# Kernel tuning notes

Measured on AMD Instinct MI355X. Metric: run time of the kernel, lower is better.

## Reference

```python
import jax, jax.numpy as jnp
import numpy as np

POOL_RATIO = 0.25
ROUTING_NUM = 3
B, N, D, H = 32, 2048, 512, 512


def setup_inputs() -> dict:
    key = jax.random.key(0)
    k_x, k_adj, k_w = jax.random.split(key, 3)
    x = jax.random.normal(k_x, (B, N, D), dtype=jnp.float32)
    # variable node counts per graph; row 0 uses all N nodes so max_cluster is static
    rng = np.random.default_rng(0)
    lens = np.full(B, N, dtype=np.int64)
    lens[1:] = rng.integers(N // 2, N + 1, size=B - 1)
    mask_np = (np.arange(N)[None, :] < lens[:, None])  # [B,N] bool
    mask = jnp.asarray(mask_np)
    # sparse-ish random adjacency, zeroed outside the node mask
    adj = (jax.random.uniform(k_adj, (B, N, N)) < 0.01).astype(jnp.float32)
    m = mask.astype(jnp.float32)
    adj = adj * m[:, None, :] * m[:, :, None]
    W = jax.random.normal(k_w, (D, H), dtype=jnp.float32) * 0.02
    b = jnp.zeros((H,), dtype=jnp.float32)
    return {"x": x, "adj": adj, "W": W, "b": b, "mask": mask}


def masked_softmax(s, m):
    # m: bool broadcastable to s; masked entries -> exactly 0 probability
    s = jnp.where(m, s, jnp.float32(-1e9))
    return jax.nn.softmax(s, axis=-1) * m


def squash(s):
    # squash along last (feature) dim, as in torch sum(dim=2) on [B,C,H]
    mag_sq = jnp.sum(s * s, axis=-1, keepdims=True)
    mag = jnp.sqrt(mag_sq)
    return mag_sq / (1.0 + mag_sq) * (s / mag)


def reference(x, adj, W, b, mask):
    fmask = mask.astype(x.dtype)
    node_num = fmask.sum(axis=1)                               # [B]
    cluster_num = jnp.floor(node_num * POOL_RATIO).astype(jnp.int32)
    max_cluster = int(x.shape[1] * POOL_RATIO)                 # static (row 0 has N nodes)
    cmask = jnp.arange(max_cluster)[None, :] < cluster_num[:, None]  # [B,C] bool
    cm = cmask[:, None, :]                                     # [B,1,C]
    # embed: dense GCN layer  z = relu(adj @ x @ W + b)  -> [B,N,H]
    z = jax.nn.relu(jnp.einsum('bnm,bmd,dh->bnh', adj, x, W) + b)
    s = jax.random.normal(jax.random.key(42), (x.shape[0], x.shape[1], max_cluster), dtype=x.dtype)
    for _ in range(ROUTING_NUM):
        s = masked_softmax(s, cm)                              # [B,N,C]
        xnext = squash(jnp.einsum('bnc,bnh->bch', s, z))       # [B,C,H]
        s = s + jnp.einsum('bnh,bch->bnc', z, xnext)           # routing update
    return masked_softmax(s, cm)
```

## Files before the change

### kernel.cpp

```cpp
#include <hip/hip_runtime.h>
#include <cstdint>
#include <cstddef>

#define NB 32
#define NN 2048
#define ND 512
#define NH 512
#define NC 512
#define ROWS (NB*NN)

typedef __attribute__((ext_vector_type(8))) short short8v;
typedef __attribute__((ext_vector_type(4))) float f32x4;

#define MFMA16(a,b,c) __builtin_amdgcn_mfma_f32_16x16x32_bf16((a),(b),(c),0,0,0)

typedef const __attribute__((address_space(1))) unsigned int* gas_t;
typedef __attribute__((address_space(3))) unsigned int* las_t;

__device__ __forceinline__ void gload16(const void* g, void* l){
  __builtin_amdgcn_global_load_lds((gas_t)g, (las_t)l, 16, 0, 0);
}

__device__ __forceinline__ void fsplit(float v, unsigned short& h, unsigned short& l){
  unsigned u = __float_as_uint(v);
  unsigned hb = (u + 0x7FFFu + ((u>>16)&1u)) >> 16;
  float hf = __uint_as_float(hb<<16);
  float r = v - hf;
  unsigned ur = __float_as_uint(r);
  l = (unsigned short)((ur + 0x7FFFu + ((ur>>16)&1u)) >> 16);
  h = (unsigned short)hb;
}

__device__ __forceinline__ unsigned rotl32(unsigned x, int d){ return (x<<d)|(x>>(32-d)); }

__device__ __forceinline__ unsigned threefry_xor(unsigned k0, unsigned k1, unsigned c0, unsigned c1){
  unsigned ks2 = 0x1BD11BDAu ^ k0 ^ k1;
  unsigned x0 = c0 + k0, x1 = c1 + k1;
#define TF_RND(r) { x0 += x1; x1 = rotl32(x1,(r)); x1 ^= x0; }
  TF_RND(13) TF_RND(15) TF_RND(26) TF_RND(6)
  x0 += k1;  x1 += ks2 + 1u;
  TF_RND(17) TF_RND(29) TF_RND(16) TF_RND(24)
  x0 += ks2; x1 += k0 + 2u;
  TF_RND(13) TF_RND(15) TF_RND(26) TF_RND(6)
  x0 += k0;  x1 += k1 + 3u;
  TF_RND(17) TF_RND(29) TF_RND(16) TF_RND(24)
  x0 += k1;  x1 += ks2 + 4u;
  TF_RND(13) TF_RND(15) TF_RND(26) TF_RND(6)
  x0 += ks2; x1 += k0 + 5u;
#undef TF_RND
  return x0 ^ x1;
}

__device__ __forceinline__ float bits_to_normal(unsigned bits){
  float f = __uint_as_float((bits >> 9) | 0x3f800000u) - 1.0f;
  const float lo = -0.99999994f;
  float u = fmaxf(lo, fmaf(f, 2.0f, lo));
  float w = -log1pf(-(u*u));
  float p;
  if (w < 5.0f){
    w -= 2.5f;
    p =            2.81022636e-08f;
    p = fmaf(p, w, 3.43273939e-07f);
    p = fmaf(p, w, -3.5233877e-06f);
    p = fmaf(p, w, -4.39150654e-06f);
    p = fmaf(p, w, 0.00021858087f);
    p = fmaf(p, w, -0.00125372503f);
    p = fmaf(p, w, -0.00417768164f);
    p = fmaf(p, w, 0.246640727f);
    p = fmaf(p, w, 1.50140941f);
  } else {
    w = sqrtf(w) - 3.0f;
    p =            -0.000200214257f;
    p = fmaf(p, w, 0.000100950558f);
    p = fmaf(p, w, 0.00134934322f);
    p = fmaf(p, w, -0.00367342844f);
    p = fmaf(p, w, 0.00573950773f);
    p = fmaf(p, w, -0.0076224613f);
    p = fmaf(p, w, 0.00943887047f);
    p = fmaf(p, w, 1.00167406f);
    p = fmaf(p, w, 2.83297682f);
  }
  return 1.4142135623730951f * (p * u);
}

__global__ void __launch_bounds__(256) rng_kernel(float* __restrict__ s){
  unsigned i = blockIdx.x * 256u + threadIdx.x;
  s[i] = bits_to_normal(threefry_xor(0u, 42u, 0u, i));
}

__global__ void __launch_bounds__(256) counts_kernel(const unsigned char* __restrict__ mraw,
                                                     int* __restrict__ cnum){
  __shared__ int red[256];
  int b = blockIdx.x, tid = threadIdx.x;
  unsigned char b0 = mraw[0], b1 = mraw[1];
  int cnt = 0;
  if (b0 == 1 && b1 == 1){
    const unsigned char* p = mraw + (size_t)b * NN;
    for (int i = tid; i < NN; i += 256) cnt += (p[i] != 0);
  } else if (b0 == 1){
    const int* p = (const int*)mraw + (size_t)b * NN;
    for (int i = tid; i < NN; i += 256) cnt += (p[i] != 0);
  } else {
    const float* p = (const float*)mraw + (size_t)b * NN;
    for (int i = tid; i < NN; i += 256) cnt += (p[i] != 0.0f);
  }
  red[tid] = cnt; __syncthreads();
  for (int off = 128; off; off >>= 1){ if (tid < off) red[tid] += red[tid+off]; __syncthreads(); }
  if (tid == 0) cnum[b] = red[0] >> 2;
}

__global__ void __launch_bounds__(256) spmm_kernel(const float* __restrict__ adj,
                                                   const float* __restrict__ x,
                                                   unsigned short* __restrict__ yh,
                                                   unsigned short* __restrict__ yl){
  __shared__ int   idxs[NN];
  __shared__ float vals[NN];
  __shared__ int   scan[256];
  int row = blockIdx.x;
  int b = row >> 11;
  int tid = threadIdx.x;
  const float* arow = adj + (size_t)row * NN;
  float v[8];
  *(float4*)&v[0] = *(const float4*)(arow + tid*8);
  *(float4*)&v[4] = *(const float4*)(arow + tid*8 + 4);
  int lc = 0;
  #pragma unroll
  for (int j=0;j<8;j++) lc += (v[j] != 0.0f);
  scan[tid] = lc; __syncthreads();
  for (int off=1; off<256; off<<=1){
    int t = (tid >= off) ? scan[tid-off] : 0;
    __syncthreads();
    scan[tid] += t;
    __syncthreads();
  }
  int pos = scan[tid] - lc;
  int total = scan[255];
  #pragma unroll
  for (int j=0;j<8;j++){
    if (v[j] != 0.0f){ idxs[pos] = tid*8 + j; vals[pos] = v[j]; pos++; }
  }
  __syncthreads();
  float acc0 = 0.f, acc1 = 0.f;
  const float* xb = x + (size_t)b * NN * ND;
  for (int j=0;j<total;j++){
    int m = idxs[j]; float a = vals[j];
    acc0 = fmaf(a, xb[(size_t)m*ND + tid      ], acc0);
    acc1 = fmaf(a, xb[(size_t)m*ND + tid + 256], acc1);
  }
  unsigned short h,l;
  size_t base = (size_t)row * ND;
  fsplit(acc0,h,l); yh[base+tid]=h;     yl[base+tid]=l;
  fsplit(acc1,h,l); yh[base+tid+256]=h; yl[base+tid+256]=l;
}

__global__ void __launch_bounds__(256) wsplit_kernel(const float* __restrict__ W,
                                                     unsigned short* __restrict__ WTh,
                                                     unsigned short* __restrict__ WTl){
  __shared__ float t[32][33];
  int bx = blockIdx.x, by = blockIdx.y;
  int x = threadIdx.x & 31, y = threadIdx.x >> 5;
  for (int yy=y; yy<32; yy+=8) t[yy][x] = W[(size_t)(bx*32+yy)*512 + by*32 + x];
  __syncthreads();
  for (int yy=y; yy<32; yy+=8){
    float v = t[x][yy];
    unsigned short h,l; fsplit(v,h,l);
    size_t idx = (size_t)(by*32+yy)*512 + bx*32 + x;
    WTh[idx]=h; WTl[idx]=l;
  }
}

template<bool SPLIT>
__global__ void __launch_bounds__(256) softmax_kernel(float* __restrict__ s,
                                                      unsigned short* __restrict__ sh,
                                                      unsigned short* __restrict__ sl,
                                                      const int* __restrict__ cnum){
  int row  = blockIdx.x*4 + (threadIdx.x >> 6);
  int lane = threadIdx.x & 63;
  int b = row >> 11;
  int Kc = cnum[b];
  float* p = s + (size_t)row * NC;
  float4 v0 = *(const float4*)(p + lane*4);
  float4 v1 = *(const float4*)(p + lane*4 + 256);
  float e[8] = {v0.x,v0.y,v0.z,v0.w,v1.x,v1.y,v1.z,v1.w};
  float m = -3.0e38f;
  #pragma unroll
  for (int j=0;j<8;j++){
    int c = (j<4) ? lane*4 + j : lane*4 + 252 + j;
    if (c < Kc) m = fmaxf(m, e[j]);
  }
  #pragma unroll
  for (int off=32; off; off>>=1) m = fmaxf(m, __shfl_xor(m, off, 64));
  float r[8]; float sum = 0.f;
  #pragma unroll
  for (int j=0;j<8;j++){
    int c = (j<4) ? lane*4 + j : lane*4 + 252 + j;
    r[j] = (c < Kc) ? expf(e[j] - m) : 0.0f;
    sum += r[j];
  }
  #pragma unroll
  for (int off=32; off; off>>=1) sum += __shfl_xor(sum, off, 64);
  float inv = 1.0f / sum;
  #pragma unroll
  for (int j=0;j<8;j++) r[j] *= inv;
  *(float4*)(p + lane*4)       = make_float4(r[0],r[1],r[2],r[3]);
  *(float4*)(p + lane*4 + 256) = make_float4(r[4],r[5],r[6],r[7]);
  if constexpr (SPLIT){
    unsigned long long ph=0, pl=0, qh=0, ql=0;
    #pragma unroll
    for (int j=0;j<4;j++){
      unsigned short h,l;
      fsplit(r[j],h,l);
      ph |= (unsigned long long)h << (16*j);  pl |= (unsigned long long)l << (16*j);
      fsplit(r[4+j],h,l);
      qh |= (unsigned long long)h << (16*j);  ql |= (unsigned long long)l << (16*j);
    }
    size_t base = (size_t)row * NC + lane*4;
    *(unsigned long long*)(sh + base)       = ph;
    *(unsigned long long*)(sl + base)       = pl;
    *(unsigned long long*)(sh + base + 256) = qh;
    *(unsigned long long*)(sl + base + 256) = ql;
  }
}

template<int EPI>
__global__ void __launch_bounds__(512,2) gemm256_kernel(
    const unsigned short* __restrict__ Ah, const unsigned short* __restrict__ Al,
    const unsigned short* __restrict__ Bh, const unsigned short* __restrict__ Bl,
    unsigned short* __restrict__ OutH, unsigned short* __restrict__ OutL,
    float* __restrict__ Cf, const float* __restrict__ S2,
    const float* __restrict__ bias, const float* __restrict__ scale,
    int K, long sA, long sB, long sC)
{
  __shared__ __align__(16) unsigned char smem[131072];
  int bz = blockIdx.z;
  Ah += (size_t)bz*sA; Al += (size_t)bz*sA;
  Bh += (size_t)bz*sB; Bl += (size_t)bz*sB;
  if constexpr (EPI==2){ Cf += (size_t)bz*sC; S2 += (size_t)bz*sC; scale += (size_t)bz*NC; }
  int m0 = blockIdx.x*256, n0 = blockIdx.y*256;
  int tid = threadIdx.x;
  int l = tid & 63, wid = tid >> 6;
  int wr = wid >> 2, wc = wid & 3;
  int lr = l & 15, lk = l >> 4;

  int offA[8], offB[4];
  #pragma unroll
  for (int i=0;i<8;i++){
    int ra = wr*128 + i*16 + lr;
    offA[i] = ra*64 + ((lk ^ ((ra>>1)&3))<<4);
  }
  #pragma unroll
  for (int j=0;j<4;j++){
    int rb = wc*64 + j*16 + lr;
    offB[j] = rb*64 + ((lk ^ ((rb>>1)&3))<<4);
  }

  int srow = tid >> 2;
  int gslot = (tid & 3) ^ ((srow>>1)&3);
  const unsigned short* gA0 = Ah + (size_t)(m0 +       srow)*512 + gslot*8;
  const unsigned short* gA1 = Ah + (size_t)(m0 + 128 + srow)*512 + gslot*8;
  const unsigned short* gA2 = Al + (size_t)(m0 +       srow)*512 + gslot*8;
  const unsigned short* gA3 = Al + (size_t)(m0 + 128 + srow)*512 + gslot*8;
  const unsigned short* gB0 = Bh + (size_t)(n0 +       srow)*512 + gslot*8;
  const unsigned short* gB1 = Bh + (size_t)(n0 + 128 + srow)*512 + gslot*8;
  const unsigned short* gB2 = Bl + (size_t)(n0 +       srow)*512 + gslot*8;
  const unsigned short* gB3 = Bl + (size_t)(n0 + 128 + srow)*512 + gslot*8;

  f32x4 acc[8][4] = {};

#define STAGE256(buf, k0) { \
    unsigned char* db = smem + (buf)*65536 + wid*1024; \
    gload16(gA0 + (k0), db);          gload16(gA1 + (k0), db + 8192); \
    gload16(gA2 + (k0), db + 16384);  gload16(gA3 + (k0), db + 24576); \
    gload16(gB0 + (k0), db + 32768);  gload16(gB1 + (k0), db + 40960); \
    gload16(gB2 + (k0), db + 49152);  gload16(gB3 + (k0), db + 57344); }

  STAGE256(0, 0)
  __syncthreads();
  int KT = K >> 5;
  for (int t = 0; t < KT; ++t){
    if (t+1 < KT) STAGE256((t+1)&1, (t+1)*32)
    const unsigned char* base = smem + (t&1)*65536;
    short8v ah[8], bh[4], bl[4];
    #pragma unroll
    for (int i=0;i<8;i++) ah[i] = *(const short8v*)(base + offA[i]);
    #pragma unroll
    for (int j=0;j<4;j++){
      bh[j] = *(const short8v*)(base + 32768 + offB[j]);
      bl[j] = *(const short8v*)(base + 49152 + offB[j]);
    }
    #pragma unroll
    for (int i=0;i<8;i++)
      #pragma unroll
      for (int j=0;j<4;j++) acc[i][j] = MFMA16(ah[i], bh[j], acc[i][j]);
    #pragma unroll
    for (int i=0;i<8;i++)
      #pragma unroll
      for (int j=0;j<4;j++) acc[i][j] = MFMA16(ah[i], bl[j], acc[i][j]);
    #pragma unroll
    for (int i=0;i<8;i++){
      short8v al = *(const short8v*)(base + 16384 + offA[i]);
      #pragma unroll
      for (int j=0;j<4;j++) acc[i][j] = MFMA16(al, bh[j], acc[i][j]);
    }
    __syncthreads();
  }
#undef STAGE256

  float aux[4];
  #pragma unroll
  for (int j=0;j<4;j++){
    int gcol = n0 + wc*64 + j*16 + lr;
    if constexpr (EPI==1) aux[j] = bias[gcol];
    if constexpr (EPI==2) aux[j] = scale[gcol];
  }
  #pragma unroll
  for (int i=0;i<8;i++){
    #pragma unroll
    for (int r=0;r<4;r++){
      int grow = m0 + wr*128 + i*16 + lk*4 + r;
      size_t rowb = (size_t)grow*512 + n0 + wc*64 + lr;
      #pragma unroll
      for (int j=0;j<4;j++){
        float v = acc[i][j][r];
        if constexpr (EPI==1){
          v = fmaxf(v + aux[j], 0.f);
          unsigned short h,lo2; fsplit(v,h,lo2);
          OutH[rowb + j*16] = h; OutL[rowb + j*16] = lo2;
        } else {
          Cf[rowb + j*16] = S2[rowb + j*16] + aux[j]*v;
        }
      }
    }
  }
}

__global__ void __launch_bounds__(512,2) gemmT256_kernel(
    const unsigned short* __restrict__ Ah, const unsigned short* __restrict__ Al,
    const unsigned short* __restrict__ Bh, const unsigned short* __restrict__ Bl,
    unsigned short* __restrict__ OutH, unsigned short* __restrict__ OutL,
    float* __restrict__ parts, int K)
{
  __shared__ __align__(16) unsigned char smem[98304];
  int bz = blockIdx.z;
  size_t boff = (size_t)bz * NN * 512;
  Ah += boff; Al += boff; Bh += boff; Bl += boff;
  int m0 = blockIdx.x*256, n0 = blockIdx.y*128;
  int tid = threadIdx.x;
  int l = tid & 63, wid = tid >> 6;
  int wr = wid >> 2, wc = wid & 3;
  int lr = l & 15, lk = l >> 4;

  int offA[8], offB[2];
  #pragma unroll
  for (int i=0;i<8;i++){
    int ra = wr*128 + i*16 + lr;
    offA[i] = ra*64 + ((lk ^ ((ra>>1)&3) ^ ((ra>>3)&3))<<4);
  }
  #pragma unroll
  for (int j=0;j<2;j++){
    int rb = wc*32 + j*16 + lr;
    offB[j] = rb*64 + ((lk ^ ((rb>>1)&3) ^ ((rb>>3)&3))<<4);
  }

  int np  = tid & 15;
  int seg = tid >> 4;
  f32x4 acc[8][2] = {};

  short8v ra0h, ra1h, ra0l, ra1l, rb0h, rb1h, rb0l, rb1l;
  int have_b = (tid < 256);

#define TLOAD(k0) { \
    size_t ga = (size_t)((k0) + 2*np)*512 + m0 + seg*8; \
    ra0h = *(const short8v*)(Ah + ga); ra1h = *(const short8v*)(Ah + ga + 512); \
    ra0l = *(const short8v*)(Al + ga); ra1l = *(const short8v*)(Al + ga + 512); \
    if (have_b){ \
      size_t gb = (size_t)((k0) + 2*np)*512 + n0 + seg*8; \
      rb0h = *(const short8v*)(Bh + gb); rb1h = *(const short8v*)(Bh + gb + 512); \
      rb0l = *(const short8v*)(Bl + gb); rb1l = *(const short8v*)(Bl + gb + 512); } }

#define TWRITE(buf) { \
    unsigned char* bb = smem + (buf)*49152; \
    _Pragma("unroll") \
    for (int k=0;k<8;k++){ \
      int c = seg*8 + k; \
      int ps = (np>>2) ^ ((c>>1)&3) ^ ((c>>3)&3); \
      int byo = c*64 + ps*16 + (np&3)*4; \
      *(unsigned int*)(bb + byo)         = (unsigned int)(unsigned short)ra0h[k] | ((unsigned int)(unsigned short)ra1h[k]<<16); \
      *(unsigned int*)(bb + 16384 + byo) = (unsigned int)(unsigned short)ra0l[k] | ((unsigned int)(unsigned short)ra1l[k]<<16); \
      if (have_b){ \
        *(unsigned int*)(bb + 32768 + byo) = (unsigned int)(unsigned short)rb0h[k] | ((unsigned int)(unsigned short)rb1h[k]<<16); \
        *(unsigned int*)(bb + 40960 + byo) = (unsigned int)(unsigned short)rb0l[k] | ((unsigned int)(unsigned short)rb1l[k]<<16); } } }

  TLOAD(0)
  TWRITE(0)
  __syncthreads();
  int KT = K >> 5;
  for (int t = 0; t < KT; ++t){
    int more = (t+1 < KT);
    if (more) TLOAD((t+1)*32)
    const unsigned char* base = smem + (t&1)*49152;
    short8v ah[8], bh[2], bl[2];
    #pragma unroll
    for (int i=0;i<8;i++) ah[i] = *(const short8v*)(base + offA[i]);
    #pragma unroll
    for (int j=0;j<2;j++){
      bh[j] = *(const short8v*)(base + 32768 + offB[j]);
      bl[j] = *(const short8v*)(base + 40960 + offB[j]);
    }
    #pragma unroll
    for (int i=0;i<8;i++)
      #pragma unroll
      for (int j=0;j<2;j++) acc[i][j] = MFMA16(ah[i], bh[j], acc[i][j]);
    #pragma unroll
    for (int i=0;i<8;i++)
      #pragma unroll
      for (int j=0;j<2;j++) acc[i][j] = MFMA16(ah[i], bl[j], acc[i][j]);
    #pragma unroll
    for (int i=0;i<8;i++){
      short8v al = *(const short8v*)(base + 16384 + offA[i]);
      #pragma unroll
      for (int j=0;j<2;j++) acc[i][j] = MFMA16(al, bh[j], acc[i][j]);
    }
    if (more) TWRITE((t+1)&1)
    __syncthreads();
  }
#undef TLOAD
#undef TWRITE

  #pragma unroll
  for (int i=0;i<8;i++){
    #pragma unroll
    for (int r=0;r<4;r++){
      int grow = m0 + wr*128 + i*16 + lk*4 + r;
      float p = 0.f;
      size_t rowb = (size_t)bz*NC*NH + (size_t)grow*512 + n0 + wc*32 + lr;
      #pragma unroll
      for (int j=0;j<2;j++){
        float v = acc[i][j][r];
        p = fmaf(v,v,p);
        unsigned short h,lo2; fsplit(v,h,lo2);
        OutH[rowb + j*16] = h; OutL[rowb + j*16] = lo2;
      }
      p += __shfl_xor(p, 1, 64);
      p += __shfl_xor(p, 2, 64);
      p += __shfl_xor(p, 4, 64);
      p += __shfl_xor(p, 8, 64);
      if (lr == 0) parts[(((size_t)bz*NC) + grow)*16 + blockIdx.y*4 + wc] = p;
    }
  }
}

__global__ void __launch_bounds__(512) scale_kernel(const float* __restrict__ parts,
                                                    float* __restrict__ scale){
  int b = blockIdx.x, c = threadIdx.x;
  const float* p = parts + ((size_t)b*NC + c)*16;
  float m2 = 0.f;
  #pragma unroll
  for (int j=0;j<16;j++) m2 += p[j];
  float sc = 0.0f;
  if (m2 > 0.0f) sc = (m2/(1.0f+m2)) / sqrtf(m2);
  scale[(size_t)b*NC + c] = sc;
}

extern "C" void kernel_launch(void* const* d_in, const int* in_sizes, int n_in,
                              void* d_out, int out_size, void* d_ws, size_t ws_size,
                              hipStream_t stream) {
  const float* x    = (const float*)d_in[0];
  const float* adj  = (const float*)d_in[1];
  const float* W    = (const float*)d_in[2];
  const float* bias = (const float*)d_in[3];
  const unsigned char* mask = (const unsigned char*)d_in[4];
  float* out = (float*)d_out;
  char* ws = (char*)d_ws;

  unsigned short* zh   = (unsigned short*)(ws);
  unsigned short* zl   = (unsigned short*)(ws + 67108864);
  unsigned short* sth  = (unsigned short*)(ws + 134217728);
  unsigned short* stl  = (unsigned short*)(ws + 201326592);
  unsigned short* xnh  = (unsigned short*)(ws + 268435456);
  unsigned short* xnl  = (unsigned short*)(ws + 285212672);
  unsigned short* WTh  = (unsigned short*)(ws + 301989888);
  unsigned short* WTl  = (unsigned short*)(ws + 302514176);
  float* parts         = (float*)(ws + 303038464);
  float* scalebuf      = (float*)(ws + 304087040);
  int*   cnum          = (int*)(ws + 304152576);
  unsigned short* yh = sth;
  unsigned short* yl = stl;

  counts_kernel<<<NB, 256, 0, stream>>>(mask, cnum);
  wsplit_kernel<<<dim3(16,16), 256, 0, stream>>>(W, WTh, WTl);
  spmm_kernel<<<ROWS, 256, 0, stream>>>(adj, x, yh, yl);
  gemm256_kernel<1><<<dim3(256,2,1), 512, 0, stream>>>(
      yh, yl, WTh, WTl, zh, zl, nullptr, nullptr, bias, nullptr, ND, 0, 0, 0);
  rng_kernel<<<(ROWS*NC)/256, 256, 0, stream>>>(out);

  for (int it = 0; it < 3; ++it){
    softmax_kernel<true><<<ROWS/4, 256, 0, stream>>>(out, sth, stl, cnum);
    gemmT256_kernel<<<dim3(2,4,NB), 512, 0, stream>>>(
        sth, stl, zh, zl, xnh, xnl, parts, NN);
    scale_kernel<<<NB, 512, 0, stream>>>(parts, scalebuf);
    gemm256_kernel<2><<<dim3(8,2,NB), 512, 0, stream>>>(
        zh, zl, xnh, xnl, nullptr, nullptr, out, out, nullptr, scalebuf,
        NH, (long)NN*NH, (long)NC*NH, (long)NN*NC);
  }
  softmax_kernel<false><<<ROWS/4, 256, 0, stream>>>(out, nullptr, nullptr, cnum);
}
```

Before: 1.485 ms.

## Skip masked rows and clusters in GEMMs, drop fp32 softmax writes, swizzle grids

```diff
diff --git a/kernel.cpp b/kernel.cpp
--- a/kernel.cpp
+++ b/kernel.cpp
@@ -89,7 +89,8 @@
 }
 
 __global__ void __launch_bounds__(256) counts_kernel(const unsigned char* __restrict__ mraw,
-                                                     int* __restrict__ cnum){
+                                                     int* __restrict__ cnum,
+                                                     int* __restrict__ lenbuf){
   __shared__ int red[256];
   int b = blockIdx.x, tid = threadIdx.x;
   unsigned char b0 = mraw[0], b1 = mraw[1];
@@ -106,19 +107,26 @@
   }
   red[tid] = cnt; __syncthreads();
   for (int off = 128; off; off >>= 1){ if (tid < off) red[tid] += red[tid+off]; __syncthreads(); }
-  if (tid == 0) cnum[b] = red[0] >> 2;
+  if (tid == 0){ cnum[b] = red[0] >> 2; lenbuf[b] = red[0]; }
 }
 
 __global__ void __launch_bounds__(256) spmm_kernel(const float* __restrict__ adj,
                                                    const float* __restrict__ x,
                                                    unsigned short* __restrict__ yh,
-                                                   unsigned short* __restrict__ yl){
+                                                   unsigned short* __restrict__ yl,
+                                                   const int* __restrict__ lenbuf){
   __shared__ int   idxs[NN];
   __shared__ float vals[NN];
   __shared__ int   scan[256];
   int row = blockIdx.x;
   int b = row >> 11;
+  int n = row & 2047;
   int tid = threadIdx.x;
+  size_t base = (size_t)row * ND;
+  if (n >= lenbuf[b]){
+    yh[base+tid]=0; yl[base+tid]=0; yh[base+tid+256]=0; yl[base+tid+256]=0;
+    return;
+  }
   const float* arow = adj + (size_t)row * NN;
   float v[8];
   *(float4*)&v[0] = *(const float4*)(arow + tid*8);
@@ -148,7 +156,6 @@
     acc1 = fmaf(a, xb[(size_t)m*ND + tid + 256], acc1);
   }
   unsigned short h,l;
-  size_t base = (size_t)row * ND;
   fsplit(acc0,h,l); yh[base+tid]=h;     yl[base+tid]=l;
   fsplit(acc1,h,l); yh[base+tid+256]=h; yl[base+tid+256]=l;
 }
@@ -169,7 +176,7 @@
   }
 }
 
-template<bool SPLIT>
+template<bool SPLIT, bool WF32>
 __global__ void __launch_bounds__(256) softmax_kernel(float* __restrict__ s,
                                                       unsigned short* __restrict__ sh,
                                                       unsigned short* __restrict__ sl,
@@ -202,8 +209,10 @@
   float inv = 1.0f / sum;
   #pragma unroll
   for (int j=0;j<8;j++) r[j] *= inv;
-  *(float4*)(p + lane*4)       = make_float4(r[0],r[1],r[2],r[3]);
-  *(float4*)(p + lane*4 + 256) = make_float4(r[4],r[5],r[6],r[7]);
+  if constexpr (WF32){
+    *(float4*)(p + lane*4)       = make_float4(r[0],r[1],r[2],r[3]);
+    *(float4*)(p + lane*4 + 256) = make_float4(r[4],r[5],r[6],r[7]);
+  }
   if constexpr (SPLIT){
     unsigned long long ph=0, pl=0, qh=0, ql=0;
     #pragma unroll
@@ -222,36 +231,57 @@
   }
 }
 
-template<int EPI>
+template<int EPI, bool SWZ>
 __global__ void __launch_bounds__(512,2) gemm256_kernel(
     const unsigned short* __restrict__ Ah, const unsigned short* __restrict__ Al,
     const unsigned short* __restrict__ Bh, const unsigned short* __restrict__ Bl,
     unsigned short* __restrict__ OutH, unsigned short* __restrict__ OutL,
-    float* __restrict__ Cf, const float* __restrict__ S2,
+    float* __restrict__ Cf, const unsigned short* __restrict__ S2h,
+    const unsigned short* __restrict__ S2l,
     const float* __restrict__ bias, const float* __restrict__ scale,
+    const int* __restrict__ lenbuf, const int* __restrict__ cnumbuf,
     int K, long sA, long sB, long sC)
 {
   __shared__ __align__(16) unsigned char smem[131072];
-  int bz = blockIdx.z;
+  int bx, by, bz;
+  if constexpr (SWZ){
+    int flat = blockIdx.x;
+    int f2 = (flat & 7)*64 + (flat >> 3);
+    bz = f2 >> 4; int rem = f2 & 15; bx = rem >> 1; by = rem & 1;
+  } else { bx = blockIdx.x; by = blockIdx.y; bz = blockIdx.z; }
   Ah += (size_t)bz*sA; Al += (size_t)bz*sA;
   Bh += (size_t)bz*sB; Bl += (size_t)bz*sB;
-  if constexpr (EPI==2){ Cf += (size_t)bz*sC; S2 += (size_t)bz*sC; scale += (size_t)bz*NC; }
-  int m0 = blockIdx.x*256, n0 = blockIdx.y*256;
+  if constexpr (EPI==2){
+    Cf += (size_t)bz*sC; S2h += (size_t)bz*sC; S2l += (size_t)bz*sC;
+    scale += (size_t)bz*NC;
+  }
+  int m0 = bx*256, n0 = by*256;
+  int lim_m, lim_n;
+  if constexpr (EPI==1){
+    lim_m = lenbuf[m0 >> 11] - (m0 & 2047);
+    lim_n = 256;
+  } else {
+    lim_m = lenbuf[bz] - m0;
+    lim_n = cnumbuf[bz] - n0;
+  }
   int tid = threadIdx.x;
   int l = tid & 63, wid = tid >> 6;
   int wr = wid >> 2, wc = wid & 3;
   int lr = l & 15, lk = l >> 4;
 
+  bool liA[8]; bool liB[4];
   int offA[8], offB[4];
   #pragma unroll
   for (int i=0;i<8;i++){
     int ra = wr*128 + i*16 + lr;
     offA[i] = ra*64 + ((lk ^ ((ra>>1)&3))<<4);
+    liA[i] = (wr*128 + i*16) < lim_m;
   }
   #pragma unroll
   for (int j=0;j<4;j++){
     int rb = wc*64 + j*16 + lr;
     offB[j] = rb*64 + ((lk ^ ((rb>>1)&3))<<4);
+    liB[j] = (wc*64 + j*16) < lim_n;
   }
 
   int srow = tid >> 2;
@@ -282,25 +312,25 @@
     const unsigned char* base = smem + (t&1)*65536;
     short8v ah[8], bh[4], bl[4];
     #pragma unroll
-    for (int i=0;i<8;i++) ah[i] = *(const short8v*)(base + offA[i]);
-    #pragma unroll
-    for (int j=0;j<4;j++){
+    for (int i=0;i<8;i++) if (liA[i]) ah[i] = *(const short8v*)(base + offA[i]);
+    #pragma unroll
+    for (int j=0;j<4;j++) if (liB[j]){
       bh[j] = *(const short8v*)(base + 32768 + offB[j]);
       bl[j] = *(const short8v*)(base + 49152 + offB[j]);
     }
     #pragma unroll
-    for (int i=0;i<8;i++)
-      #pragma unroll
-      for (int j=0;j<4;j++) acc[i][j] = MFMA16(ah[i], bh[j], acc[i][j]);
-    #pragma unroll
-    for (int i=0;i<8;i++)
-      #pragma unroll
-      for (int j=0;j<4;j++) acc[i][j] = MFMA16(ah[i], bl[j], acc[i][j]);
-    #pragma unroll
-    for (int i=0;i<8;i++){
+    for (int i=0;i<8;i++) if (liA[i])
+      #pragma unroll
+      for (int j=0;j<4;j++) if (liB[j]) acc[i][j] = MFMA16(ah[i], bh[j], acc[i][j]);
+    #pragma unroll
+    for (int i=0;i<8;i++) if (liA[i])
+      #pragma unroll
+      for (int j=0;j<4;j++) if (liB[j]) acc[i][j] = MFMA16(ah[i], bl[j], acc[i][j]);
+    #pragma unroll
+    for (int i=0;i<8;i++) if (liA[i]){
       short8v al = *(const short8v*)(base + 16384 + offA[i]);
       #pragma unroll
-      for (int j=0;j<4;j++) acc[i][j] = MFMA16(al, bh[j], acc[i][j]);
+      for (int j=0;j<4;j++) if (liB[j]) acc[i][j] = MFMA16(al, bh[j], acc[i][j]);
     }
     __syncthreads();
   }
@@ -327,7 +357,9 @@
           unsigned short h,lo2; fsplit(v,h,lo2);
           OutH[rowb + j*16] = h; OutL[rowb + j*16] = lo2;
         } else {
-          Cf[rowb + j*16] = S2[rowb + j*16] + aux[j]*v;
+          unsigned hh = S2h[rowb + j*16], ll = S2l[rowb + j*16];
+          float s2 = __uint_as_float(hh<<16) + __uint_as_float(ll<<16);
+          Cf[rowb + j*16] = s2 + aux[j]*v;
         }
       }
     }
@@ -338,23 +370,30 @@
     const unsigned short* __restrict__ Ah, const unsigned short* __restrict__ Al,
     const unsigned short* __restrict__ Bh, const unsigned short* __restrict__ Bl,
     unsigned short* __restrict__ OutH, unsigned short* __restrict__ OutL,
-    float* __restrict__ parts, int K)
+    float* __restrict__ parts, const int* __restrict__ lenbuf,
+    const int* __restrict__ cnumbuf)
 {
   __shared__ __align__(16) unsigned char smem[98304];
-  int bz = blockIdx.z;
+  int flat = blockIdx.x;
+  int f2 = (flat & 7)*32 + (flat >> 3);
+  int bz = f2 >> 3; int rem = f2 & 7; int bx = rem & 1; int by = rem >> 1;
   size_t boff = (size_t)bz * NN * 512;
   Ah += boff; Al += boff; Bh += boff; Bl += boff;
-  int m0 = blockIdx.x*256, n0 = blockIdx.y*128;
+  int m0 = bx*256, n0 = by*128;
+  int KT = (lenbuf[bz] + 31) >> 5;
+  int limc = cnumbuf[bz] - m0;
   int tid = threadIdx.x;
   int l = tid & 63, wid = tid >> 6;
   int wr = wid >> 2, wc = wid & 3;
   int lr = l & 15, lk = l >> 4;
 
+  bool liA[8];
   int offA[8], offB[2];
   #pragma unroll
   for (int i=0;i<8;i++){
     int ra = wr*128 + i*16 + lr;
     offA[i] = ra*64 + ((lk ^ ((ra>>1)&3) ^ ((ra>>3)&3))<<4);
+    liA[i] = (wr*128 + i*16) < limc;
   }
   #pragma unroll
   for (int j=0;j<2;j++){
@@ -394,29 +433,28 @@
   TLOAD(0)
   TWRITE(0)
   __syncthreads();
-  int KT = K >> 5;
   for (int t = 0; t < KT; ++t){
     int more = (t+1 < KT);
     if (more) TLOAD((t+1)*32)
     const unsigned char* base = smem + (t&1)*49152;
     short8v ah[8], bh[2], bl[2];
     #pragma unroll
-    for (int i=0;i<8;i++) ah[i] = *(const short8v*)(base + offA[i]);
+    for (int i=0;i<8;i++) if (liA[i]) ah[i] = *(const short8v*)(base + offA[i]);
     #pragma unroll
     for (int j=0;j<2;j++){
       bh[j] = *(const short8v*)(base + 32768 + offB[j]);
       bl[j] = *(const short8v*)(base + 40960 + offB[j]);
     }
     #pragma unroll
-    for (int i=0;i<8;i++)
+    for (int i=0;i<8;i++) if (liA[i])
       #pragma unroll
       for (int j=0;j<2;j++) acc[i][j] = MFMA16(ah[i], bh[j], acc[i][j]);
     #pragma unroll
-    for (int i=0;i<8;i++)
+    for (int i=0;i<8;i++) if (liA[i])
       #pragma unroll
       for (int j=0;j<2;j++) acc[i][j] = MFMA16(ah[i], bl[j], acc[i][j]);
     #pragma unroll
-    for (int i=0;i<8;i++){
+    for (int i=0;i<8;i++) if (liA[i]){
       short8v al = *(const short8v*)(base + 16384 + offA[i]);
       #pragma unroll
       for (int j=0;j<2;j++) acc[i][j] = MFMA16(al, bh[j], acc[i][j]);
@@ -445,7 +483,7 @@
       p += __shfl_xor(p, 2, 64);
       p += __shfl_xor(p, 4, 64);
       p += __shfl_xor(p, 8, 64);
-      if (lr == 0) parts[(((size_t)bz*NC) + grow)*16 + blockIdx.y*4 + wc] = p;
+      if (lr == 0) parts[(((size_t)bz*NC) + grow)*16 + by*4 + wc] = p;
     }
   }
 }
@@ -484,24 +522,26 @@
   float* parts         = (float*)(ws + 303038464);
   float* scalebuf      = (float*)(ws + 304087040);
   int*   cnum          = (int*)(ws + 304152576);
+  int*   lenbuf        = (int*)(ws + 304152704);
   unsigned short* yh = sth;
   unsigned short* yl = stl;
 
-  counts_kernel<<<NB, 256, 0, stream>>>(mask, cnum);
+  counts_kernel<<<NB, 256, 0, stream>>>(mask, cnum, lenbuf);
   wsplit_kernel<<<dim3(16,16), 256, 0, stream>>>(W, WTh, WTl);
-  spmm_kernel<<<ROWS, 256, 0, stream>>>(adj, x, yh, yl);
-  gemm256_kernel<1><<<dim3(256,2,1), 512, 0, stream>>>(
-      yh, yl, WTh, WTl, zh, zl, nullptr, nullptr, bias, nullptr, ND, 0, 0, 0);
+  spmm_kernel<<<ROWS, 256, 0, stream>>>(adj, x, yh, yl, lenbuf);
+  gemm256_kernel<1,false><<<dim3(256,2,1), 512, 0, stream>>>(
+      yh, yl, WTh, WTl, zh, zl, nullptr, nullptr, nullptr, bias, nullptr,
+      lenbuf, cnum, ND, 0, 0, 0);
   rng_kernel<<<(ROWS*NC)/256, 256, 0, stream>>>(out);
 
   for (int it = 0; it < 3; ++it){
-    softmax_kernel<true><<<ROWS/4, 256, 0, stream>>>(out, sth, stl, cnum);
-    gemmT256_kernel<<<dim3(2,4,NB), 512, 0, stream>>>(
-        sth, stl, zh, zl, xnh, xnl, parts, NN);
+    softmax_kernel<true,false><<<ROWS/4, 256, 0, stream>>>(out, sth, stl, cnum);
+    gemmT256_kernel<<<256, 512, 0, stream>>>(
+        sth, stl, zh, zl, xnh, xnl, parts, lenbuf, cnum);
     scale_kernel<<<NB, 512, 0, stream>>>(parts, scalebuf);
-    gemm256_kernel<2><<<dim3(8,2,NB), 512, 0, stream>>>(
-        zh, zl, xnh, xnl, nullptr, nullptr, out, out, nullptr, scalebuf,
-        NH, (long)NN*NH, (long)NC*NH, (long)NN*NC);
-  }
-  softmax_kernel<false><<<ROWS/4, 256, 0, stream>>>(out, nullptr, nullptr, cnum);
-}
+    gemm256_kernel<2,true><<<512, 512, 0, stream>>>(
+        zh, zl, xnh, xnl, nullptr, nullptr, out, sth, stl, nullptr, scalebuf,
+        lenbuf, cnum, NH, (long)NN*NH, (long)NC*NH, (long)NN*NC);
+  }
+  softmax_kernel<false,true><<<ROWS/4, 256, 0, stream>>>(out, nullptr, nullptr, cnum);
+}
```

Measured after the change: 1.467 ms. No clear change (-1.2%).
